# Kernel tuning notes

Hardware: AMD Instinct MI355X
Metric: run time of the kernel (lower is better)

The kernel has to match this reference:

```python
import jax, jax.numpy as jnp
import numpy as np

B, T, F, H = 64, 512, 128, 512

def _rnn(x_seq, h0, Wih, Whh, bih, bhh):
    # PyTorch vanilla RNN: h_t = tanh(x_t @ Wih^T + bih + h_{t-1} @ Whh^T + bhh)
    def step(h, x_t):
        h = jnp.tanh(x_t @ Wih.T + bih + h @ Whh.T + bhh)
        return h, h
    _, ys = jax.lax.scan(step, h0, jnp.swapaxes(x_seq, 0, 1))  # scan over time
    return jnp.swapaxes(ys, 0, 1)  # [B, T, H]

def _decode(z, Wih, Whh, bih, bhh):
    # decoder input at step t = concat(prev_output, z_t); 1-layer RNN so prev_output == h_{t-1}
    def step(h, z_t):
        u = jnp.concatenate([h, z_t], axis=-1)  # [B, 2H]
        h_new = jnp.tanh(u @ Wih.T + bih + h @ Whh.T + bhh)
        return h_new, h_new
    h0 = jnp.zeros((z.shape[0], Whh.shape[0]), z.dtype)
    _, ys = jax.lax.scan(step, h0, jnp.swapaxes(z, 0, 1))
    return jnp.swapaxes(ys, 0, 1)  # [B, T, H]

def setup_inputs() -> dict:
    key = jax.random.key(0)
    ks = jax.random.split(key, 16)
    s = 0.02
    p = {
        'x':   jax.random.normal(ks[0], (B, T, F), jnp.float32),
        'eps': jax.random.normal(ks[1], (B, T, H), jnp.float32),
        'Wih_en': jax.random.normal(ks[2], (H, F)) * s,
        'Whh_en': jax.random.normal(ks[3], (H, H)) * s,
        'bih_en': jax.random.normal(ks[4], (H,)) * s,
        'bhh_en': jax.random.normal(ks[5], (H,)) * s,
        'W_mu':  jax.random.normal(ks[6], (H, H)) * s,
        'b_mu':  jax.random.normal(ks[7], (H,)) * s,
        'W_lv':  jax.random.normal(ks[8], (H, H)) * s,
        'b_lv':  jax.random.normal(ks[9], (H,)) * s,
        'Wih_de': jax.random.normal(ks[10], (H, 2 * H)) * s,
        'Whh_de': jax.random.normal(ks[11], (H, H)) * s,
        'bih_de': jax.random.normal(ks[12], (H,)) * s,
        'bhh_de': jax.random.normal(ks[13], (H,)) * s,
        'W_mux': jax.random.normal(ks[14], (F, H)) * s,
        'b_mux': jnp.zeros((F,)),
        'W_lvx': jax.random.normal(ks[15], (F, H)) * s,
        'b_lvx': jnp.zeros((F,)),
    }
    return p

def reference(x, eps, Wih_en, Whh_en, bih_en, bhh_en, W_mu, b_mu, W_lv, b_lv,
              Wih_de, Whh_de, bih_de, bhh_de, W_mux, b_mux, W_lvx, b_lvx):
    h0 = jnp.zeros((x.shape[0], Whh_en.shape[0]), x.dtype)
    y = _rnn(x, h0, Wih_en, Whh_en, bih_en, bhh_en)                 # [B,T,H]
    mu_post = y @ W_mu.T + b_mu
    logsigma2_post = y @ W_lv.T + b_lv
    z = eps * jnp.exp(logsigma2_post / 2) + mu_post                 # reparameterize
    outputs = _decode(z, Wih_de, Whh_de, bih_de, bhh_de)            # [B,T,H]
    mu_xhat = outputs @ W_mux.T + b_mux
    logsigma2_xhat = outputs @ W_lvx.T + b_lvx
    return (mu_post, logsigma2_post, mu_xhat, logsigma2_xhat)
```

## Files before the change

kernel.cpp:

```cpp
#include <hip/hip_runtime.h>

typedef _Float16 h2_t __attribute__((ext_vector_type(2)));
typedef _Float16 h4_t __attribute__((ext_vector_type(4)));
typedef _Float16 h8_t __attribute__((ext_vector_type(8)));
typedef float    f4_t __attribute__((ext_vector_type(4)));

#define B_  64
#define T_  512
#define F_  128
#define H_  512

static __device__ __forceinline__ float fdot2f(h2_t a, h2_t b, float c) {
#if __has_builtin(__builtin_amdgcn_fdot2)
    return __builtin_amdgcn_fdot2(a, b, c, false);
#else
    return c + (float)a.x * (float)b.x + (float)a.y * (float)b.y;
#endif
}

static __device__ __forceinline__ void dot8(float& acc, uint4 w, uint4 h) {
    acc = fdot2f(__builtin_bit_cast(h2_t, w.x), __builtin_bit_cast(h2_t, h.x), acc);
    acc = fdot2f(__builtin_bit_cast(h2_t, w.y), __builtin_bit_cast(h2_t, h.y), acc);
    acc = fdot2f(__builtin_bit_cast(h2_t, w.z), __builtin_bit_cast(h2_t, h.z), acc);
    acc = fdot2f(__builtin_bit_cast(h2_t, w.w), __builtin_bit_cast(h2_t, h.w), acc);
}

static __device__ __forceinline__ int d4(int acc, unsigned a, unsigned b) {
#if __has_builtin(__builtin_amdgcn_sdot4)
    return __builtin_amdgcn_sdot4((int)a, (int)b, acc, false);
#else
    #pragma unroll
    for (int i = 0; i < 4; ++i)
        acc += (int)(signed char)((a >> (8 * i)) & 0xff) *
               (int)(signed char)((b >> (8 * i)) & 0xff);
    return acc;
#endif
}
static __device__ __forceinline__ int dot16i8(int acc, uint4 w, uint4 h) {
    acc = d4(acc, w.x, h.x);
    acc = d4(acc, w.y, h.y);
    acc = d4(acc, w.z, h.z);
    acc = d4(acc, w.w, h.w);
    return acc;
}

__global__ void k_cast_f16(const float* __restrict__ src, _Float16* __restrict__ dst, int n) {
    int i = blockIdx.x * blockDim.x + threadIdx.x;
    if (i < n) dst[i] = (_Float16)src[i];
}

__global__ void k_prep_z(const float* __restrict__ Wih_de, _Float16* __restrict__ Wz) {
    int i = blockIdx.x * blockDim.x + threadIdx.x;
    int cc = i >> 9, kk = i & 511;
    Wz[i] = (_Float16)Wih_de[cc * 1024 + 512 + kk];
}

__global__ void k_prep_bias(const float* __restrict__ a, const float* __restrict__ b,
                            float* __restrict__ o) {
    int i = threadIdx.x;
    o[i] = a[i] + b[i];
}

__global__ void k_quant(const float* __restrict__ A, int sA,
                        const float* __restrict__ Bo, int sB,
                        signed char* __restrict__ q, float* __restrict__ fac) {
    __shared__ float red[128];
    const int c = blockIdx.x, t = threadIdx.x;
    f4_t v = *(const f4_t*)(A + (size_t)c * sA + t * 4);
    if (Bo) {
        f4_t vb = *(const f4_t*)(Bo + (size_t)c * sB + t * 4);
        v = v + vb;
    }
    float m = fmaxf(fmaxf(fabsf(v[0]), fabsf(v[1])), fmaxf(fabsf(v[2]), fabsf(v[3])));
    red[t] = m;
    __syncthreads();
    for (int o = 64; o; o >>= 1) {
        if (t < o) red[t] = fmaxf(red[t], red[t + o]);
        __syncthreads();
    }
    float mx = red[0];
    float inv = mx > 0.f ? 127.f / mx : 0.f;
    unsigned r = 0;
    #pragma unroll
    for (int i = 0; i < 4; ++i) {
        int qi = (int)rintf(fminf(fmaxf(v[i] * inv, -127.f), 127.f));
        r |= ((unsigned)(unsigned char)(signed char)qi) << (8 * i);
    }
    *(unsigned*)(q + (size_t)c * 512 + t * 4) = r;
    if (t == 0) fac[c] = mx > 0.f ? mx / 127.f : 0.f;
}

#define BM 128
#define BN 128
#define BK 32
#define LDT 40

__global__ __launch_bounds__(256) void k_gemm(
    const _Float16* __restrict__ A, const _Float16* __restrict__ Bt,
    const float* __restrict__ bias,
    float* __restrict__ Cf, _Float16* __restrict__ Ch,
    int M, int N, int K) {
    __shared__ _Float16 Al[BM * LDT];
    __shared__ _Float16 Bl[BN * LDT];
    const int tid = threadIdx.x;
    const int bm = blockIdx.x * BM, bn = blockIdx.y * BN;
    const int wid = tid >> 6, lane = tid & 63;
    const int wm = (wid >> 1) * 64, wn = (wid & 1) * 64;
    const int l15 = lane & 15, l4 = lane >> 4;

    f4_t acc[4][4];
    #pragma unroll
    for (int i = 0; i < 4; ++i)
        #pragma unroll
        for (int j = 0; j < 4; ++j) {
            f4_t zz = {0.f, 0.f, 0.f, 0.f};
            acc[i][j] = zz;
        }

    const int r = tid >> 1, hf = tid & 1;
    const h8_t* gA0 = (const h8_t*)(A + (size_t)(bm + r) * K);
    const h8_t* gB0 = (const h8_t*)(Bt + (size_t)(bn + r) * K);

    for (int k0 = 0; k0 < K; k0 += BK) {
        __syncthreads();
        int kf = (k0 >> 3) + hf * 2;
        h8_t a0 = gA0[kf], a1 = gA0[kf + 1];
        h8_t b0 = gB0[kf], b1 = gB0[kf + 1];
        *(h8_t*)&Al[r * LDT + hf * 16]     = a0;
        *(h8_t*)&Al[r * LDT + hf * 16 + 8] = a1;
        *(h8_t*)&Bl[r * LDT + hf * 16]     = b0;
        *(h8_t*)&Bl[r * LDT + hf * 16 + 8] = b1;
        __syncthreads();
        h8_t af[4], bf[4];
        #pragma unroll
        for (int i = 0; i < 4; ++i) af[i] = *(const h8_t*)&Al[(wm + i * 16 + l15) * LDT + l4 * 8];
        #pragma unroll
        for (int j = 0; j < 4; ++j) bf[j] = *(const h8_t*)&Bl[(wn + j * 16 + l15) * LDT + l4 * 8];
        #pragma unroll
        for (int i = 0; i < 4; ++i)
            #pragma unroll
            for (int j = 0; j < 4; ++j)
                acc[i][j] = __builtin_amdgcn_mfma_f32_16x16x32_f16(af[i], bf[j], acc[i][j], 0, 0, 0);
    }

    #pragma unroll
    for (int i = 0; i < 4; ++i) {
        int m0 = bm + wm + i * 16 + l4 * 4;
        #pragma unroll
        for (int j = 0; j < 4; ++j) {
            int n0 = bn + wn + j * 16 + l15;
            float bb = bias ? bias[n0] : 0.f;
            #pragma unroll
            for (int rr = 0; rr < 4; ++rr) {
                float v = acc[i][j][rr] + bb;
                size_t off = (size_t)(m0 + rr) * N + n0;
                if (Cf) Cf[off] = v;
                if (Ch) Ch[off] = (_Float16)v;
            }
        }
    }
}

__global__ __launch_bounds__(512) void k_rnn(
    const signed char* __restrict__ Wq,
    const float* __restrict__ fac,
    const _Float16* __restrict__ pre,
    _Float16* __restrict__ out) {
    __shared__ __align__(16) uint4 WL[4 * 512];
    __shared__ __align__(16) signed char h_q[H_];
    __shared__ int ipart[H_];

    const int tid = threadIdx.x;
    const int c2 = tid & 255;
    const int s = tid >> 8;
    const int b = blockIdx.x;

    const uint4* q0 = (const uint4*)(Wq + (size_t)c2 * 512 + s * 256);
    const uint4* q1 = (const uint4*)(Wq + (size_t)(c2 + 256) * 512 + s * 256);
    uint4 wa[14], wb[14];
    #pragma unroll
    for (int j = 0; j < 14; ++j) { wa[j] = q0[j]; wb[j] = q1[j]; }
    WL[0 * 512 + tid] = q0[14];
    WL[1 * 512 + tid] = q0[15];
    WL[2 * 512 + tid] = q1[14];
    WL[3 * 512 + tid] = q1[15];
    if (tid < 32) ((uint4*)h_q)[tid] = make_uint4(0u, 0u, 0u, 0u);
    __syncthreads();

    const size_t base = (size_t)b * T_ * H_ + tid;
    float pcur = (float)pre[base];
    const float facr = fac[tid] * (1.f / 127.f);

    for (int t = 0; t < T_; ++t) {
        int tn = (t + 1 < T_) ? t + 1 : t;
        _Float16 pnx = pre[base + (size_t)tn * H_];

        int i0 = 0, i1 = 0;
        const uint4* hv = ((const uint4*)h_q) + s * 16;
        #pragma unroll
        for (int j = 0; j < 14; ++j) {
            uint4 hh = hv[j];
            i0 = dot16i8(i0, wa[j], hh);
            i1 = dot16i8(i1, wb[j], hh);
        }
        {
            uint4 hh = hv[14];
            i0 = dot16i8(i0, WL[0 * 512 + tid], hh);
            i1 = dot16i8(i1, WL[2 * 512 + tid], hh);
        }
        {
            uint4 hh = hv[15];
            i0 = dot16i8(i0, WL[1 * 512 + tid], hh);
            i1 = dot16i8(i1, WL[3 * 512 + tid], hh);
        }

        ipart[tid ^ 256] = s ? i0 : i1;
        __syncthreads();
        int mine = s ? i1 : i0;
        float hn = tanhf((float)(mine + ipart[tid]) * facr + pcur);
        out[base + (size_t)t * H_] = (_Float16)hn;
        h_q[tid] = (signed char)(int)rintf(hn * 127.f);
        __syncthreads();
        pcur = (float)pnx;
    }
}

__global__ void k_z(const float* __restrict__ mu, const float* __restrict__ lv,
                    const float* __restrict__ eps, _Float16* __restrict__ z, int n4) {
    int i = blockIdx.x * blockDim.x + threadIdx.x;
    if (i >= n4) return;
    f4_t m = ((const f4_t*)mu)[i];
    f4_t l = ((const f4_t*)lv)[i];
    f4_t e = ((const f4_t*)eps)[i];
    h4_t r;
    #pragma unroll
    for (int j = 0; j < 4; ++j) r[j] = (_Float16)(e[j] * expf(l[j] * 0.5f) + m[j]);
    ((h4_t*)z)[i] = r;
}

extern "C" void kernel_launch(void* const* d_in, const int* in_sizes, int n_in,
                              void* d_out, int out_size, void* d_ws, size_t ws_size,
                              hipStream_t stream) {
    const float* x      = (const float*)d_in[0];
    const float* eps    = (const float*)d_in[1];
    const float* Wih_en = (const float*)d_in[2];
    const float* Whh_en = (const float*)d_in[3];
    const float* bih_en = (const float*)d_in[4];
    const float* bhh_en = (const float*)d_in[5];
    const float* W_mu   = (const float*)d_in[6];
    const float* b_mu   = (const float*)d_in[7];
    const float* W_lv   = (const float*)d_in[8];
    const float* b_lv   = (const float*)d_in[9];
    const float* Wih_de = (const float*)d_in[10];
    const float* Whh_de = (const float*)d_in[11];
    const float* bih_de = (const float*)d_in[12];
    const float* bhh_de = (const float*)d_in[13];
    const float* W_mux  = (const float*)d_in[14];
    const float* b_mux  = (const float*)d_in[15];
    const float* W_lvx  = (const float*)d_in[16];
    const float* b_lvx  = (const float*)d_in[17];
    float* out = (float*)d_out;

    char* ws = (char*)d_ws;
    _Float16* Wih_en_h = (_Float16*)(ws + 0);
    _Float16* W_mu_h   = (_Float16*)(ws + 655360);
    _Float16* W_lv_h   = (_Float16*)(ws + 1179648);
    _Float16* Wz_h     = (_Float16*)(ws + 1703936);
    _Float16* Wmux_h   = (_Float16*)(ws + 2752512);
    _Float16* Wlvx_h   = (_Float16*)(ws + 2883584);
    float*    benc     = (float*)(ws + 3014656);
    float*    bdec     = (float*)(ws + 3016704);
    signed char* Wq_en = (signed char*)(ws + 3018752);
    signed char* Wq_de = (signed char*)(ws + 3280896);
    float*    fac_en   = (float*)(ws + 3543040);
    float*    fac_de   = (float*)(ws + 3545088);
    _Float16* x_h      = (_Float16*)(ws + 4194304);
    _Float16* pre_h    = (_Float16*)(ws + 12582912);
    _Float16* act_h    = (_Float16*)(ws + 46137344);
    _Float16* z_h      = (_Float16*)(ws + 79691776);

    const int thr = 256;
    k_cast_f16<<<(65536 + thr - 1) / thr, thr, 0, stream>>>(Wih_en, Wih_en_h, 65536);
    k_cast_f16<<<(262144 + thr - 1) / thr, thr, 0, stream>>>(W_mu, W_mu_h, 262144);
    k_cast_f16<<<(262144 + thr - 1) / thr, thr, 0, stream>>>(W_lv, W_lv_h, 262144);
    k_cast_f16<<<(65536 + thr - 1) / thr, thr, 0, stream>>>(W_mux, Wmux_h, 65536);
    k_cast_f16<<<(65536 + thr - 1) / thr, thr, 0, stream>>>(W_lvx, Wlvx_h, 65536);
    k_cast_f16<<<(4194304 + thr - 1) / thr, thr, 0, stream>>>(x, x_h, 4194304);
    k_prep_z<<<262144 / thr, thr, 0, stream>>>(Wih_de, Wz_h);
    k_prep_bias<<<1, 512, 0, stream>>>(bih_en, bhh_en, benc);
    k_prep_bias<<<1, 512, 0, stream>>>(bih_de, bhh_de, bdec);
    k_quant<<<512, 128, 0, stream>>>(Whh_en, 512, nullptr, 0, Wq_en, fac_en);
    k_quant<<<512, 128, 0, stream>>>(Wih_de, 1024, Whh_de, 512, Wq_de, fac_de);

    dim3 gFull(32768 / BM, 512 / BN);
    dim3 gNarrow(32768 / BM, 1);

    k_gemm<<<gFull, 256, 0, stream>>>(x_h, Wih_en_h, benc, nullptr, pre_h, 32768, 512, 128);
    k_rnn<<<64, 512, 0, stream>>>(Wq_en, fac_en, pre_h, act_h);
    k_gemm<<<gFull, 256, 0, stream>>>(act_h, W_mu_h, b_mu, out, nullptr, 32768, 512, 512);
    k_gemm<<<gFull, 256, 0, stream>>>(act_h, W_lv_h, b_lv, out + 16777216, nullptr, 32768, 512, 512);
    k_z<<<4194304 / thr, thr, 0, stream>>>(out, out + 16777216, eps, z_h, 4194304);
    k_gemm<<<gFull, 256, 0, stream>>>(z_h, Wz_h, bdec, nullptr, pre_h, 32768, 512, 512);
    k_rnn<<<64, 512, 0, stream>>>(Wq_de, fac_de, pre_h, act_h);
    k_gemm<<<gNarrow, 256, 0, stream>>>(act_h, Wmux_h, b_mux, out + 33554432, nullptr, 32768, 128, 512);
    k_gemm<<<gNarrow, 256, 0, stream>>>(act_h, Wlvx_h, b_lvx, out + 37748736, nullptr, 32768, 128, 512);
}
```

Before: 1.144 ms.

## Split RNN recurrent matvec into four K-slices per thread with LDS reduction

The int8 recurrent matvec in k_rnn is repartitioned. Each thread now handles four output columns over a 128-wide K slice instead of two columns over a 256-wide slice. Partial sums for all four slices go to a larger LDS buffer, and each thread then sums four partials for its own output. This shortens each thread's dependent dot-product chain and exposes more independent accumulators, at the cost of more LDS writes and reads per timestep.

```diff
diff --git a/kernel.cpp b/kernel.cpp
--- a/kernel.cpp
+++ b/kernel.cpp
@@ -168,22 +168,25 @@
     _Float16* __restrict__ out) {
     __shared__ __align__(16) uint4 WL[4 * 512];
     __shared__ __align__(16) signed char h_q[H_];
-    __shared__ int ipart[H_];
+    __shared__ int ipart[4 * H_ / 1 ];
 
     const int tid = threadIdx.x;
-    const int c2 = tid & 255;
-    const int s = tid >> 8;
+    const int c = tid & 127;
+    const int s = tid >> 7;
     const int b = blockIdx.x;
 
-    const uint4* q0 = (const uint4*)(Wq + (size_t)c2 * 512 + s * 256);
-    const uint4* q1 = (const uint4*)(Wq + (size_t)(c2 + 256) * 512 + s * 256);
-    uint4 wa[14], wb[14];
-    #pragma unroll
-    for (int j = 0; j < 14; ++j) { wa[j] = q0[j]; wb[j] = q1[j]; }
-    WL[0 * 512 + tid] = q0[14];
-    WL[1 * 512 + tid] = q0[15];
-    WL[2 * 512 + tid] = q1[14];
-    WL[3 * 512 + tid] = q1[15];
+    const uint4* g0 = (const uint4*)(Wq + (size_t)(c + 0)   * 512 + s * 128);
+    const uint4* g1 = (const uint4*)(Wq + (size_t)(c + 128) * 512 + s * 128);
+    const uint4* g2 = (const uint4*)(Wq + (size_t)(c + 256) * 512 + s * 128);
+    const uint4* g3 = (const uint4*)(Wq + (size_t)(c + 384) * 512 + s * 128);
+
+    uint4 w0[7], w1[7], w2[7], w3[7];
+    #pragma unroll
+    for (int j = 0; j < 7; ++j) { w0[j] = g0[j]; w1[j] = g1[j]; w2[j] = g2[j]; w3[j] = g3[j]; }
+    WL[0 * 512 + tid] = g0[7];
+    WL[1 * 512 + tid] = g1[7];
+    WL[2 * 512 + tid] = g2[7];
+    WL[3 * 512 + tid] = g3[7];
     if (tid < 32) ((uint4*)h_q)[tid] = make_uint4(0u, 0u, 0u, 0u);
     __syncthreads();
 
@@ -195,29 +198,32 @@
         int tn = (t + 1 < T_) ? t + 1 : t;
         _Float16 pnx = pre[base + (size_t)tn * H_];
 
-        int i0 = 0, i1 = 0;
-        const uint4* hv = ((const uint4*)h_q) + s * 16;
-        #pragma unroll
-        for (int j = 0; j < 14; ++j) {
+        int i0 = 0, i1 = 0, i2 = 0, i3 = 0;
+        const uint4* hv = ((const uint4*)h_q) + s * 8;
+        #pragma unroll
+        for (int j = 0; j < 7; ++j) {
             uint4 hh = hv[j];
-            i0 = dot16i8(i0, wa[j], hh);
-            i1 = dot16i8(i1, wb[j], hh);
+            i0 = dot16i8(i0, w0[j], hh);
+            i1 = dot16i8(i1, w1[j], hh);
+            i2 = dot16i8(i2, w2[j], hh);
+            i3 = dot16i8(i3, w3[j], hh);
         }
         {
-            uint4 hh = hv[14];
+            uint4 hh = hv[7];
             i0 = dot16i8(i0, WL[0 * 512 + tid], hh);
-            i1 = dot16i8(i1, WL[2 * 512 + tid], hh);
+            i1 = dot16i8(i1, WL[1 * 512 + tid], hh);
+            i2 = dot16i8(i2, WL[2 * 512 + tid], hh);
+            i3 = dot16i8(i3, WL[3 * 512 + tid], hh);
         }
-        {
-            uint4 hh = hv[15];
-            i0 = dot16i8(i0, WL[1 * 512 + tid], hh);
-            i1 = dot16i8(i1, WL[3 * 512 + tid], hh);
-        }
-
-        ipart[tid ^ 256] = s ? i0 : i1;
-        __syncthreads();
-        int mine = s ? i1 : i0;
-        float hn = tanhf((float)(mine + ipart[tid]) * facr + pcur);
+
+        ipart[s * 512 + c]       = i0;
+        ipart[s * 512 + c + 128] = i1;
+        ipart[s * 512 + c + 256] = i2;
+        ipart[s * 512 + c + 384] = i3;
+        __syncthreads();
+
+        int tot = ipart[tid] + ipart[512 + tid] + ipart[1024 + tid] + ipart[1536 + tid];
+        float hn = tanhf((float)tot * facr + pcur);
         out[base + (size_t)t * H_] = (_Float16)hn;
         h_q[tid] = (signed char)(int)rintf(hn * 127.f);
         __syncthreads();
```

Result: slower. 1.176 ms (+2.8%).
